# Optimization experiments

Measured on AMD Instinct MI355X. Metric: run time of the kernel, lower is better.

## Reference

```python
import jax, jax.numpy as jnp
import numpy as np

B, N, K = 8, 1024, 32
C_IN, C_OUT, C_SIPF, HEADS = 128, 256, 8, 4
D_H = C_IN // HEADS
EPS = 1e-5
NEG_SLOPE = 0.2


def setup_inputs() -> dict:
    key = jax.random.key(0)
    ks = jax.random.split(key, 12)
    s = 0.05
    x = jax.random.normal(ks[0], (B, C_IN, N), jnp.float32)
    SiPF = jax.random.normal(ks[1], (B, N, K, C_SIPF), jnp.float32)
    col_local = jax.random.randint(ks[2], (B, N, K), 0, N)
    # feat_select expects GLOBAL indices (it subtracts the b*N base)
    col = (col_local + jnp.arange(B)[:, None, None] * N).reshape(-1).astype(jnp.int64)
    return {
        "x": x,
        "SiPF": SiPF,
        "w_kv": jax.random.normal(ks[3], (2 * C_IN, C_IN), jnp.float32) * s,
        "wk1": jax.random.normal(ks[4], (C_IN, C_SIPF), jnp.float32) * s,
        "bnk_gamma": jnp.ones((C_IN,), jnp.float32),
        "bnk_beta": jnp.zeros((C_IN,), jnp.float32),
        "wk2": jax.random.normal(ks[5], (C_IN, C_IN), jnp.float32) * s,
        "wv1": jax.random.normal(ks[6], (C_IN, C_SIPF), jnp.float32) * s,
        "bv1": jnp.zeros((C_IN,), jnp.float32),
        "bnv_gamma": jnp.ones((C_IN,), jnp.float32),
        "bnv_beta": jnp.zeros((C_IN,), jnp.float32),
        "wv2": jax.random.normal(ks[7], (C_IN, C_IN), jnp.float32) * s,
        "bv2": jnp.zeros((C_IN,), jnp.float32),
        "we": jax.random.normal(ks[8], (C_OUT, 2 * C_IN), jnp.float32) * s,
        "bne_gamma": jnp.ones((C_OUT,), jnp.float32),
        "bne_beta": jnp.zeros((C_OUT,), jnp.float32),
        "col": col,
        "bs": B,
    }


def _bn2d(t, gamma, beta):
    # BatchNorm2d, training mode: stats over (B, N, K) per channel
    m = t.mean(axis=(0, 2, 3), keepdims=True)
    v = t.var(axis=(0, 2, 3), keepdims=True)
    return (t - m) * jax.lax.rsqrt(v + EPS) * gamma[None, :, None, None] + beta[None, :, None, None]


def _bn1d(t, gamma, beta):
    m = t.mean(axis=(0, 2), keepdims=True)
    v = t.var(axis=(0, 2), keepdims=True)
    return (t - m) * jax.lax.rsqrt(v + EPS) * gamma[None, :, None] + beta[None, :, None]


def _feat_select(feat, col):
    # feat: [B, C, N]; col: [B*N*K] global indices -> [B, C, N, K]
    idx = col.reshape(B, N * K) - (jnp.arange(B, dtype=col.dtype) * N)[:, None]
    gathered = jax.vmap(lambda f, i: f[:, i])(feat, idx)  # [B, C, N*K]
    return gathered.reshape(feat.shape[0], feat.shape[1], N, K)


def _forward(x, SiPF, col, w_kv, wk1, bnk_gamma, bnk_beta, wk2,
             wv1, bv1, bnv_gamma, bnv_beta, wv2, bv2, we, bne_gamma, bne_beta):
    fs = _feat_select(x, col)                               # [B, C_in, N, K]
    sipf = SiPF.reshape(B, N, K, C_SIPF).transpose(0, 3, 1, 2)  # [B, C_sipf, N, K]

    qv = jnp.einsum('oc,bcnk->bonk', w_kv, fs)
    q_fs, v_fs = qv[:, :C_IN], qv[:, C_IN:]

    # bias nets on SiPF (1x1 conv -> BN -> ReLU -> 1x1 conv)
    hk = jax.nn.relu(_bn2d(jnp.einsum('oc,bcnk->bonk', wk1, sipf), bnk_gamma, bnk_beta))
    k_sipf = jnp.einsum('oc,bcnk->bonk', wk2, hk)
    hv = jnp.einsum('oc,bcnk->bonk', wv1, sipf) + bv1[None, :, None, None]
    hv = jax.nn.relu(_bn2d(hv, bnv_gamma, bnv_beta))
    v_sipf = jnp.einsum('oc,bcnk->bonk', wv2, hv) + bv2[None, :, None, None]

    def to_heads(t):  # [B, C_in, N, K] -> [B, H, N, K, d_h]
        return t.reshape(B, HEADS, D_H, N, K).transpose(0, 1, 3, 4, 2)

    q = to_heads(q_fs)
    k = to_heads(k_sipf)
    v = to_heads(v_fs) * to_heads(v_sipf)

    scale = 1.0 / np.sqrt(D_H).astype(np.float32)
    scores = jnp.einsum('bhnkd,bhnjd->bhnkj', q, k) * scale   # [B, H, N, K, K]
    attn = jax.nn.softmax(scores, axis=-1)
    out = jnp.einsum('bhnkj,bhnjd->bhnkd', attn, v)           # [B, H, N, K, d_h]

    y = out.transpose(0, 1, 4, 2, 3).reshape(B, C_IN, N, K)
    y = y.max(axis=-1)                                        # [B, C_in, N]

    z = jnp.concatenate([y - x, x], axis=1)                   # [B, 2*C_in, N]
    z = jnp.einsum('oc,bcn->bon', we, z)
    z = _bn1d(z, bne_gamma, bne_beta)
    return jnp.where(z >= 0, z, NEG_SLOPE * z)                # LeakyReLU(0.2)


def reference(x, SiPF, w_kv, wk1, bnk_gamma, bnk_beta, wk2, wv1, bv1,
              bnv_gamma, bnv_beta, wv2, bv2, we, bne_gamma, bne_beta, col, bs):
    del bs  # unused by the torch module as well
    return _forward(x, SiPF, col, w_kv, wk1, bnk_gamma, bnk_beta, wk2,
                    wv1, bv1, bnv_gamma, bnv_beta, wv2, bv2, we, bne_gamma, bne_beta)
```

## Files before the change

### kernel.cpp

```cpp
#include <hip/hip_runtime.h>

#define B_    8
#define N_    1024
#define K_    32
#define CIN   128
#define COUT  256
#define EPSF  1e-5f
#define NEG   0.2f

#define WS_MP   0
#define WS_ESUM 12288
#define WS_ESS  12544
#define WS_BK   12800
#define WS_BV   12928
#define WB_BYTE 53248
#define XT_BYTE 331776
#define Y_BYTE  2428928
#define WQB   0
#define WVB   16384
#define WK2B  32768
#define WV2B  49152
#define WEB   65536
#define WK1F  131072
#define WV1F  135168

typedef unsigned short ushort_t;
typedef unsigned int   uint_t;
typedef __attribute__((ext_vector_type(8))) short s8v;
typedef __attribute__((ext_vector_type(4))) short s4v;
typedef __attribute__((ext_vector_type(4))) float f4v;
typedef __bf16 bf16x8 __attribute__((ext_vector_type(8)));

constexpr int   P_TOT  = B_ * N_ * K_;
constexpr float INV_P  = 1.0f / (float)P_TOT;
constexpr float INV_BN = 1.0f / (float)(B_ * N_);

__device__ __forceinline__ float b2f(ushort_t u) {
    return __uint_as_float(((uint_t)u) << 16);
}
__device__ __forceinline__ ushort_t f2b(float f) {
    return __builtin_bit_cast(ushort_t, (__bf16)f);
}
__device__ __forceinline__ bf16x8 ld8(const ushort_t* p) {
    return __builtin_bit_cast(bf16x8, *(const s8v*)p);
}
__device__ __forceinline__ int qx2(int c, int k) {
    return (c * 32 + k) ^ (((c >> 1) & 7) << 3);
}

__global__ __launch_bounds__(256) void prep_kernel(
    const float* __restrict__ x, const float* __restrict__ SiPF,
    const float* __restrict__ w_kv, const float* __restrict__ wk2,
    const float* __restrict__ wv2, const float* __restrict__ we,
    float* __restrict__ ws, ushort_t* __restrict__ wb,
    ushort_t* __restrict__ xT)
{
    __shared__ float red[4][44];
    __shared__ float tile[32][129];
    const int blk = blockIdx.x;
    const int t   = threadIdx.x;

    if (blk < 256) {
        float s1[8], s2[36];
#pragma unroll
        for (int i = 0; i < 8; ++i) s1[i] = 0.f;
#pragma unroll
        for (int i = 0; i < 36; ++i) s2[i] = 0.f;
        const int tid = blk * 256 + t;
#pragma unroll
        for (int it = 0; it < P_TOT / 65536; ++it) {
            const float4* base = (const float4*)(SiPF + (size_t)(tid + it * 65536) * 8);
            float4 a = base[0], bq = base[1];
            float v[8] = {a.x, a.y, a.z, a.w, bq.x, bq.y, bq.z, bq.w};
            int idx = 0;
#pragma unroll
            for (int i = 0; i < 8; ++i) {
                s1[i] += v[i];
#pragma unroll
                for (int j = i; j < 8; ++j) s2[idx++] += v[i] * v[j];
            }
        }
#pragma unroll
        for (int i = 0; i < 8; ++i)
            for (int m = 32; m; m >>= 1) s1[i] += __shfl_xor(s1[i], m);
#pragma unroll
        for (int i = 0; i < 36; ++i)
            for (int m = 32; m; m >>= 1) s2[i] += __shfl_xor(s2[i], m);
        if ((t & 63) == 0) {
            const int w = t >> 6;
#pragma unroll
            for (int i = 0; i < 8; ++i) red[w][i] = s1[i];
#pragma unroll
            for (int i = 0; i < 36; ++i) red[w][8 + i] = s2[i];
        }
        __syncthreads();
        if (t < 44)
            ws[WS_MP + blk * 48 + t] = red[0][t] + red[1][t] + red[2][t] + red[3][t];
    } else if (blk < 512) {
        const int tb = blk - 256;
        const int b  = tb >> 5;
        const int n0 = (tb & 31) << 5;
        const int cgr = t >> 5, n = t & 31;
#pragma unroll
        for (int i = 0; i < 16; ++i) {
            const int c = cgr * 16 + i;
            tile[n][c] = x[((size_t)(b * CIN + c)) * N_ + n0 + n];
        }
        __syncthreads();
        const int nr = t >> 3, c0 = (t & 7) * 16;
        s8v o0, o1;
#pragma unroll
        for (int j = 0; j < 8; ++j) {
            o0[j] = (short)f2b(tile[nr][c0 + j]);
            o1[j] = (short)f2b(tile[nr][c0 + 8 + j]);
        }
        s8v* dst = (s8v*)(xT + ((size_t)(b * N_ + n0 + nr)) * 128 + c0);
        dst[0] = o0; dst[1] = o1;
    } else {
        if (blk == 512) {
            ws[WS_ESUM + t] = 0.f;
            ws[WS_ESS + t]  = 0.f;
        }
        const int base = (blk - 512) * 1024 + t;
#pragma unroll
        for (int i = 0; i < 4; ++i) {
            const int e = base + i * 256;
            float v;
            if (e < 32768)      v = w_kv[e];
            else if (e < 49152) v = wk2[e - 32768];
            else if (e < 65536) v = wv2[e - 49152];
            else                v = we[e - 65536];
            wb[e] = f2b(v);
        }
    }
}

__global__ __launch_bounds__(128) void prep2_kernel(
    const float* __restrict__ wk1, const float* __restrict__ wv1,
    const float* __restrict__ bnk_gamma, const float* __restrict__ bnk_beta,
    const float* __restrict__ bnv_gamma, const float* __restrict__ bnv_beta,
    float* __restrict__ ws, ushort_t* __restrict__ wb)
{
    __shared__ float red2[44];
    const int c = threadIdx.x;
    if (c < 44) {
        float s = 0.f;
        for (int bq = 0; bq < 256; ++bq) s += ws[WS_MP + bq * 48 + c];
        red2[c] = s;
    }
    __syncthreads();

    float m1[8], wkr[8], wvr[8];
#pragma unroll
    for (int s = 0; s < 8; ++s) {
        m1[s]  = red2[s] * INV_P;
        wkr[s] = wk1[c * 8 + s];
        wvr[s] = wv1[c * 8 + s];
    }
    float mk = 0.f, mv = 0.f;
#pragma unroll
    for (int s = 0; s < 8; ++s) { mk += wkr[s] * m1[s]; mv += wvr[s] * m1[s]; }
    float ek = 0.f, ev = 0.f;
#pragma unroll
    for (int s = 0; s < 8; ++s)
#pragma unroll
        for (int s2 = 0; s2 < 8; ++s2) {
            const int i = s < s2 ? s : s2;
            const int j = s < s2 ? s2 : s;
            const float m2 = red2[8 + 8 * i - (i * (i - 1)) / 2 + (j - i)] * INV_P;
            ek += wkr[s] * wkr[s2] * m2;
            ev += wvr[s] * wvr[s2] * m2;
        }
    const float Ak = bnk_gamma[c] * rsqrtf(ek - mk * mk + EPSF);
    const float Av = bnv_gamma[c] * rsqrtf(ev - mv * mv + EPSF);
    ws[WS_BK + c] = bnk_beta[c] - mk * Ak;
    ws[WS_BV + c] = bnv_beta[c] - mv * Av;
#pragma unroll
    for (int s = 0; s < 32; ++s) {
        wb[WK1F + c * 32 + s] = s < 8 ? f2b(Ak * wkr[s]) : (ushort_t)0;
        wb[WV1F + c * 32 + s] = s < 8 ? f2b(Av * wvr[s]) : (ushort_t)0;
    }
}

__global__ __launch_bounds__(512, 4) void main_kernel(
    const float* __restrict__ SiPF, const float* __restrict__ bv2,
    const int* __restrict__ col,    const float* __restrict__ ws,
    const ushort_t* __restrict__ wb, const ushort_t* __restrict__ xT,
    ushort_t* __restrict__ y)
{
    __shared__ __align__(16) ushort_t T1[2][4096];
    __shared__ __align__(16) ushort_t T2[2][4096];
    __shared__ __align__(16) ushort_t T3[2][4096];
    __shared__ __align__(16) ushort_t T4[2][4096];

    const int bid = blockIdx.x;
    const int pi  = (bid & 7) * 512 + (bid >> 3);
    const int t   = threadIdx.x;

    const int wv_ = t >> 6, l = t & 63, lr = l & 15, lg = l >> 4;
    const int cw  = wv_ * 16;
    const f4v z4 = {0.f, 0.f, 0.f, 0.f};

    const bf16x8 wa1 = ld8(&wb[WK1F + (cw + lr) * 32 + lg * 8]);
    const bf16x8 wa2 = ld8(&wb[WV1F + (cw + lr) * 32 + lg * 8]);
    bf16x8 wf[8];
    {
        const int c = cw + lr;
#pragma unroll
        for (int kt = 0; kt < 2; ++kt) {
            const int cp0 = kt * 32 + lg * 8;
            wf[kt * 4 + 0] = ld8(&wb[WK2B + c * 128 + cp0]);
            wf[kt * 4 + 1] = ld8(&wb[WV2B + c * 128 + cp0]);
            wf[kt * 4 + 2] = ld8(&wb[WQB  + c * 128 + cp0]);
            wf[kt * 4 + 3] = ld8(&wb[WVB  + c * 128 + cp0]);
        }
    }

    {
        const int p  = t >> 8;
        const int bn = pi * 2 + p;
        const int b  = bn >> 10;
        const int tt = t & 255;
        const int k  = tt & 31;
        const int cg = tt >> 5;
        if (cg < 4) {
            const int slot = (cg * 8) ^ ((k & 3) << 3);
            s8v o8 = {0, 0, 0, 0, 0, 0, 0, 0};
            if (cg == 0) {
                const float4* sp = (const float4*)(SiPF + (size_t)bn * 256 + k * 8);
                const float4 sa = sp[0], sq = sp[1];
                o8[0] = (short)f2b(sa.x); o8[1] = (short)f2b(sa.y);
                o8[2] = (short)f2b(sa.z); o8[3] = (short)f2b(sa.w);
                o8[4] = (short)f2b(sq.x); o8[5] = (short)f2b(sq.y);
                o8[6] = (short)f2b(sq.z); o8[7] = (short)f2b(sq.w);
            }
            *(s8v*)&T4[p][k * 32 + slot] = o8;
        }
        const int idxk = col[bn * K_ + k] - b * N_;
        const s8v* xrow = (const s8v*)(xT + ((size_t)(b << 10) + idxk) * 128 + cg * 16);
        const s8v f0 = xrow[0], f1 = xrow[1];
        const int base = k * 128 + cg * 16;
        const int sw   = (k & 7) << 3;
        *(s8v*)&T1[p][(base) ^ sw]     = f0;
        *(s8v*)&T1[p][(base + 8) ^ sw] = f1;
    }
    __syncthreads();

    {
        bf16x8 sb[4];
#pragma unroll
        for (int nt = 0; nt < 4; ++nt) {
            const int pp  = nt >> 1;
            const int row = (nt & 1) * 16 + lr;
            sb[nt] = ld8(&T4[pp][row * 32 + ((lg * 8) ^ ((row & 3) << 3))]);
        }
        const float4 bka = *(const float4*)&ws[WS_BK + cw + lg * 4];
        const float4 bva = *(const float4*)&ws[WS_BV + cw + lg * 4];
        const float Bk_[4] = {bka.x, bka.y, bka.z, bka.w};
        const float Bv_[4] = {bva.x, bva.y, bva.z, bva.w};
        f4v hka[4], hva[4];
#pragma unroll
        for (int nt = 0; nt < 4; ++nt) {
            hka[nt] = __builtin_amdgcn_mfma_f32_16x16x32_bf16(wa1, sb[nt], z4, 0, 0, 0);
            hva[nt] = __builtin_amdgcn_mfma_f32_16x16x32_bf16(wa2, sb[nt], z4, 0, 0, 0);
        }
#pragma unroll
        for (int nt = 0; nt < 4; ++nt) {
            const int pp  = nt >> 1;
            const int c0  = cw + lg * 4;
            const int kc  = (nt & 1) * 16 + lr;
            const int idx = (kc * 128 + c0) ^ ((kc & 7) << 3);
            s4v hk4, hv4;
#pragma unroll
            for (int r = 0; r < 4; ++r) {
                hk4[r] = (short)f2b(fmaxf(hka[nt][r] + Bk_[r], 0.f));
                hv4[r] = (short)f2b(fmaxf(hva[nt][r] + Bv_[r], 0.f));
            }
            *(s4v*)&T2[pp][idx] = hk4;
            *(s4v*)&T3[pp][idx] = hv4;
        }
    }
    __syncthreads();

    f4v ck[4], cs[4], aq[4], av[4];
#pragma unroll
    for (int nt = 0; nt < 4; ++nt) { ck[nt] = z4; cs[nt] = z4; aq[nt] = z4; av[nt] = z4; }
#pragma unroll
    for (int kt = 0; kt < 4; ++kt) {
        const int cp0 = kt * 32 + lg * 8;
        bf16x8 bk[4], bv[4], bfr[4];
#pragma unroll
        for (int nt = 0; nt < 4; ++nt) {
            const int pp  = nt >> 1;
            const int kk_ = (nt & 1) * 16 + lr;
            const int idx = (kk_ * 128 + cp0) ^ ((lr & 7) << 3);
            bk[nt]  = ld8(&T2[pp][idx]);
            bv[nt]  = ld8(&T3[pp][idx]);
            bfr[nt] = ld8(&T1[pp][idx]);
        }
        const int c = cw + lr;
        const bf16x8 a1 = kt < 2 ? wf[kt * 4 + 0] : ld8(&wb[WK2B + c * 128 + cp0]);
        const bf16x8 a2 = kt < 2 ? wf[kt * 4 + 1] : ld8(&wb[WV2B + c * 128 + cp0]);
        const bf16x8 a3 = kt < 2 ? wf[kt * 4 + 2] : ld8(&wb[WQB  + c * 128 + cp0]);
        const bf16x8 a4 = kt < 2 ? wf[kt * 4 + 3] : ld8(&wb[WVB  + c * 128 + cp0]);
#pragma unroll
        for (int nt = 0; nt < 4; ++nt) {
            ck[nt] = __builtin_amdgcn_mfma_f32_16x16x32_bf16(a1, bk[nt],  ck[nt], 0, 0, 0);
            cs[nt] = __builtin_amdgcn_mfma_f32_16x16x32_bf16(a2, bv[nt],  cs[nt], 0, 0, 0);
            aq[nt] = __builtin_amdgcn_mfma_f32_16x16x32_bf16(a3, bfr[nt], aq[nt], 0, 0, 0);
            av[nt] = __builtin_amdgcn_mfma_f32_16x16x32_bf16(a4, bfr[nt], av[nt], 0, 0, 0);
        }
    }
#pragma unroll
    for (int nt = 0; nt < 4; ++nt) {
        const int pp  = nt >> 1;
        const int c0  = cw + lg * 4;
        const int kk_ = (nt & 1) * 16 + lr;
        const int idx = (kk_ * 128 + c0) ^ ((kk_ & 7) << 3);
        s4v ck4;
#pragma unroll
        for (int r = 0; r < 4; ++r) ck4[r] = (short)f2b(ck[nt][r]);
        *(s4v*)&T4[pp][idx] = ck4;
    }
    __syncthreads();

    {
        const float4 bvv = *(const float4*)&bv2[cw + lg * 4];
        const float bv2_[4] = {bvv.x, bvv.y, bvv.z, bvv.w};
        const float SC = 0.17677669529663687f;
#pragma unroll
        for (int nt = 0; nt < 4; ++nt) {
            const int pp  = nt >> 1;
            const int c0  = cw + lg * 4;
            const int kk_ = (nt & 1) * 16 + lr;
            const int idx = (kk_ * 128 + c0) ^ ((kk_ & 7) << 3);
            s4v q4;
#pragma unroll
            for (int r = 0; r < 4; ++r) {
                q4[r] = (short)f2b(aq[nt][r] * SC);
                T3[pp][qx2(c0 + r, kk_)] =
                    f2b(av[nt][r] * (cs[nt][r] + bv2_[r]));
            }
            *(s4v*)&T2[pp][idx] = q4;
        }
    }
    __syncthreads();

    {
        const int pp = wv_ >> 2;
        const int h  = wv_ & 3;
        const int bn = pi * 2 + pp;
        bf16x8 aqf[2], bkf[2];
#pragma unroll
        for (int mt = 0; mt < 2; ++mt)
            aqf[mt] = ld8(&T2[pp][((mt * 16 + lr) * 128 + h * 32 + lg * 8) ^ ((lr & 7) << 3)]);
#pragma unroll
        for (int nt = 0; nt < 2; ++nt)
            bkf[nt] = ld8(&T4[pp][((nt * 16 + lr) * 128 + h * 32 + lg * 8) ^ ((lr & 7) << 3)]);
        f4v s[2][2];
#pragma unroll
        for (int mt = 0; mt < 2; ++mt)
#pragma unroll
            for (int nt = 0; nt < 2; ++nt)
                s[mt][nt] = __builtin_amdgcn_mfma_f32_16x16x32_bf16(aqf[mt], bkf[nt], z4, 0, 0, 0);

        float rm[2][4], rs[2][4];
#pragma unroll
        for (int mt = 0; mt < 2; ++mt)
#pragma unroll
            for (int r = 0; r < 4; ++r)
                rm[mt][r] = fmaxf(s[mt][0][r], s[mt][1][r]);
#pragma unroll
        for (int m = 1; m <= 8; m <<= 1)
#pragma unroll
            for (int mt = 0; mt < 2; ++mt)
#pragma unroll
                for (int r = 0; r < 4; ++r)
                    rm[mt][r] = fmaxf(rm[mt][r], __shfl_xor(rm[mt][r], m));
#pragma unroll
        for (int mt = 0; mt < 2; ++mt)
#pragma unroll
            for (int nt = 0; nt < 2; ++nt)
#pragma unroll
                for (int r = 0; r < 4; ++r)
                    s[mt][nt][r] = __expf(s[mt][nt][r] - rm[mt][r]);
#pragma unroll
        for (int mt = 0; mt < 2; ++mt)
#pragma unroll
            for (int r = 0; r < 4; ++r)
                rs[mt][r] = s[mt][0][r] + s[mt][1][r];
#pragma unroll
        for (int m = 1; m <= 8; m <<= 1)
#pragma unroll
            for (int mt = 0; mt < 2; ++mt)
#pragma unroll
                for (int r = 0; r < 4; ++r)
                    rs[mt][r] += __shfl_xor(rs[mt][r], m);
#pragma unroll
        for (int mt = 0; mt < 2; ++mt)
#pragma unroll
            for (int r = 0; r < 4; ++r)
                rs[mt][r] = 1.0f / rs[mt][r];

        ushort_t* P = &T1[pp][h * 1024];
#pragma unroll
        for (int mt = 0; mt < 2; ++mt)
#pragma unroll
            for (int nt = 0; nt < 2; ++nt)
#pragma unroll
                for (int r = 0; r < 4; ++r) {
                    const int kq = mt * 16 + lg * 4 + r;
                    const int j  = nt * 16 + lr;
                    P[(kq * 32 + j) ^ ((kq & 7) << 3)] = f2b(s[mt][nt][r] * rs[mt][r]);
                }

        bf16x8 af[2], pb[2];
#pragma unroll
        for (int mt2 = 0; mt2 < 2; ++mt2)
            af[mt2] = ld8(&T3[pp][qx2(h * 32 + mt2 * 16 + lr, lg * 8)]);
#pragma unroll
        for (int nt2 = 0; nt2 < 2; ++nt2) {
            const int kq2 = nt2 * 16 + lr;
            pb[nt2] = ld8(&P[(kq2 * 32 + lg * 8) ^ ((lr & 7) << 3)]);
        }
        f4v o2[2][2];
#pragma unroll
        for (int mt2 = 0; mt2 < 2; ++mt2)
#pragma unroll
            for (int nt2 = 0; nt2 < 2; ++nt2)
                o2[mt2][nt2] = __builtin_amdgcn_mfma_f32_16x16x32_bf16(af[mt2], pb[nt2], z4, 0, 0, 0);

        float ym[2][4];
#pragma unroll
        for (int mt2 = 0; mt2 < 2; ++mt2)
#pragma unroll
            for (int r = 0; r < 4; ++r)
                ym[mt2][r] = fmaxf(o2[mt2][0][r], o2[mt2][1][r]);
#pragma unroll
        for (int m = 1; m <= 8; m <<= 1)
#pragma unroll
            for (int mt2 = 0; mt2 < 2; ++mt2)
#pragma unroll
                for (int r = 0; r < 4; ++r)
                    ym[mt2][r] = fmaxf(ym[mt2][r], __shfl_xor(ym[mt2][r], m));
        if (lr == 0) {
#pragma unroll
            for (int mt2 = 0; mt2 < 2; ++mt2) {
                unsigned long long pk = 0;
#pragma unroll
                for (int r = 0; r < 4; ++r)
                    pk |= ((unsigned long long)f2b(ym[mt2][r])) << (16 * r);
                *(unsigned long long*)&y[(size_t)bn * 128 + h * 32 + mt2 * 16 + lg * 4] = pk;
            }
        }
    }
}

__global__ __launch_bounds__(256) void zgemm_kernel(
    const ushort_t* __restrict__ wb, const ushort_t* __restrict__ xT,
    const ushort_t* __restrict__ y, float* __restrict__ ws,
    float* __restrict__ out)
{
    __shared__ __align__(16) ushort_t Bt[32 * 256];
    const int blk = blockIdx.x;
    const int bn0 = (blk >> 1) * 32;
    const int mh  = (blk & 1) * 128;
    const int t   = threadIdx.x;
    {
        const int r   = t >> 3;
        const int c0  = (t & 7) * 16;
        const int bnr = bn0 + r;
        const s8v* yr = (const s8v*)(y  + (size_t)bnr * 128 + c0);
        const s8v* xr = (const s8v*)(xT + (size_t)bnr * 128 + c0);
        const s8v y0 = yr[0], y1 = yr[1], x0 = xr[0], x1 = xr[1];
        s8v d0, d1;
#pragma unroll
        for (int j = 0; j < 8; ++j) {
            d0[j] = (short)f2b(b2f((ushort_t)y0[j]) - b2f((ushort_t)x0[j]));
            d1[j] = (short)f2b(b2f((ushort_t)y1[j]) - b2f((ushort_t)x1[j]));
        }
        const int sw = (r & 7) << 3;
        *(s8v*)&Bt[(r * 256 + c0) ^ sw]           = d0;
        *(s8v*)&Bt[(r * 256 + c0 + 8) ^ sw]       = d1;
        *(s8v*)&Bt[(r * 256 + 128 + c0) ^ sw]     = x0;
        *(s8v*)&Bt[(r * 256 + 128 + c0 + 8) ^ sw] = x1;
    }
    __syncthreads();

    const int w = t >> 6, l = t & 63, lr = l & 15, lg = l >> 4;
    const f4v z4 = {0.f, 0.f, 0.f, 0.f};
    f4v acc[2][2];
#pragma unroll
    for (int mt = 0; mt < 2; ++mt)
#pragma unroll
        for (int nt = 0; nt < 2; ++nt) acc[mt][nt] = z4;

#pragma unroll
    for (int kt = 0; kt < 8; ++kt) {
        const int kc = kt * 32 + lg * 8;
        bf16x8 bf[2];
#pragma unroll
        for (int nt = 0; nt < 2; ++nt) {
            const int rl = nt * 16 + lr;
            bf[nt] = ld8(&Bt[(rl * 256 + kc) ^ ((lr & 7) << 3)]);
        }
#pragma unroll
        for (int mt = 0; mt < 2; ++mt) {
            const int o = mh + w * 32 + mt * 16 + lr;
            const bf16x8 am = ld8(&wb[WEB + o * 256 + kc]);
#pragma unroll
            for (int nt = 0; nt < 2; ++nt)
                acc[mt][nt] = __builtin_amdgcn_mfma_f32_16x16x32_bf16(am, bf[nt], acc[mt][nt], 0, 0, 0);
        }
    }

    float sm[2][4], sq[2][4];
#pragma unroll
    for (int mt = 0; mt < 2; ++mt)
#pragma unroll
        for (int r = 0; r < 4; ++r) {
            const float a0 = acc[mt][0][r], a1 = acc[mt][1][r];
            sm[mt][r] = a0 + a1;
            sq[mt][r] = a0 * a0 + a1 * a1;
        }
#pragma unroll
    for (int m = 1; m <= 8; m <<= 1)
#pragma unroll
        for (int mt = 0; mt < 2; ++mt)
#pragma unroll
            for (int r = 0; r < 4; ++r) {
                sm[mt][r] += __shfl_xor(sm[mt][r], m);
                sq[mt][r] += __shfl_xor(sq[mt][r], m);
            }
    if (lr == 0) {
#pragma unroll
        for (int mt = 0; mt < 2; ++mt)
#pragma unroll
            for (int r = 0; r < 4; ++r) {
                const int o = mh + w * 32 + mt * 16 + lg * 4 + r;
                atomicAdd(&ws[WS_ESUM + o], sm[mt][r]);
                atomicAdd(&ws[WS_ESS + o],  sq[mt][r]);
            }
    }
    const int b = bn0 >> 10;
#pragma unroll
    for (int mt = 0; mt < 2; ++mt)
#pragma unroll
        for (int r = 0; r < 4; ++r) {
            const int o = mh + w * 32 + mt * 16 + lg * 4 + r;
#pragma unroll
            for (int nt = 0; nt < 2; ++nt) {
                const int n = (bn0 + nt * 16 + lr) & (N_ - 1);
                out[((size_t)(b * COUT + o)) * N_ + n] = acc[mt][nt][r];
            }
        }
}

__global__ __launch_bounds__(256) void apply_kernel(
    const float* __restrict__ ws, const float* __restrict__ gamma,
    const float* __restrict__ beta, float* __restrict__ out)
{
    const int bo = blockIdx.x;
    const int o  = bo & 255;
    const int b  = bo >> 8;
    const float mean = ws[WS_ESUM + o] * INV_BN;
    const float var  = ws[WS_ESS + o] * INV_BN - mean * mean;
    const float A  = gamma[o] * rsqrtf(var + EPSF);
    const float Bb = beta[o] - mean * A;
    float4* p = (float4*)(out + ((size_t)(b * COUT + o)) * N_);
    float4 v = p[threadIdx.x];
    float r0 = A * v.x + Bb, r1 = A * v.y + Bb;
    float r2 = A * v.z + Bb, r3 = A * v.w + Bb;
    v.x = r0 >= 0.f ? r0 : NEG * r0;
    v.y = r1 >= 0.f ? r1 : NEG * r1;
    v.z = r2 >= 0.f ? r2 : NEG * r2;
    v.w = r3 >= 0.f ? r3 : NEG * r3;
    p[threadIdx.x] = v;
}

extern "C" void kernel_launch(void* const* d_in, const int* in_sizes, int n_in,
                              void* d_out, int out_size, void* d_ws, size_t ws_size,
                              hipStream_t stream)
{
    (void)in_sizes; (void)n_in; (void)out_size; (void)ws_size;

    const float* x         = (const float*)d_in[0];
    const float* SiPF      = (const float*)d_in[1];
    const float* w_kv      = (const float*)d_in[2];
    const float* wk1       = (const float*)d_in[3];
    const float* bnk_gamma = (const float*)d_in[4];
    const float* bnk_beta  = (const float*)d_in[5];
    const float* wk2       = (const float*)d_in[6];
    const float* wv1       = (const float*)d_in[7];
    const float* bnv_gamma = (const float*)d_in[9];
    const float* bnv_beta  = (const float*)d_in[10];
    const float* wv2       = (const float*)d_in[11];
    const float* bv2       = (const float*)d_in[12];
    const float* we        = (const float*)d_in[13];
    const float* bne_gamma = (const float*)d_in[14];
    const float* bne_beta  = (const float*)d_in[15];
    const int*   col       = (const int*)d_in[16];

    float*    ws = (float*)d_ws;
    ushort_t* wb = (ushort_t*)((char*)d_ws + WB_BYTE);
    ushort_t* xT = (ushort_t*)((char*)d_ws + XT_BYTE);
    ushort_t* y  = (ushort_t*)((char*)d_ws + Y_BYTE);

    prep_kernel<<<640, 256, 0, stream>>>(x, SiPF, w_kv, wk2, wv2, we, ws, wb, xT);
    prep2_kernel<<<1, 128, 0, stream>>>(wk1, wv1, bnk_gamma, bnk_beta,
                                        bnv_gamma, bnv_beta, ws, wb);
    main_kernel<<<4096, 512, 0, stream>>>(SiPF, bv2, col, ws, wb, xT, y);
    zgemm_kernel<<<512, 256, 0, stream>>>(wb, xT, y, ws, (float*)d_out);
    apply_kernel<<<2048, 256, 0, stream>>>(ws, bne_gamma, bne_beta,
                                           (float*)d_out);
}
```

Measured before the change: 186.9 us.

## Defer softmax normalization via ones-MFMA row sums and drop max subtraction

The attention softmax no longer subtracts the row max or normalizes with shuffle reductions. It writes unnormalized exp scores to LDS, gets row sums from an extra MFMA against a ones vector, and rescales the PV output before the max-pool. The early register preload of the weight fragments is removed in favour of loads inside the loop, which should lower register pressure. s_setprio hints are added around the MFMA-heavy sections. Dropping the max subtraction risks exp overflow if scores grow large, and the row sums are taken from bf16-rounded probabilities.

```diff
diff --git a/kernel.cpp b/kernel.cpp
--- a/kernel.cpp
+++ b/kernel.cpp
@@ -196,25 +196,6 @@
     const int bid = blockIdx.x;
     const int pi  = (bid & 7) * 512 + (bid >> 3);
     const int t   = threadIdx.x;
-
-    const int wv_ = t >> 6, l = t & 63, lr = l & 15, lg = l >> 4;
-    const int cw  = wv_ * 16;
-    const f4v z4 = {0.f, 0.f, 0.f, 0.f};
-
-    const bf16x8 wa1 = ld8(&wb[WK1F + (cw + lr) * 32 + lg * 8]);
-    const bf16x8 wa2 = ld8(&wb[WV1F + (cw + lr) * 32 + lg * 8]);
-    bf16x8 wf[8];
-    {
-        const int c = cw + lr;
-#pragma unroll
-        for (int kt = 0; kt < 2; ++kt) {
-            const int cp0 = kt * 32 + lg * 8;
-            wf[kt * 4 + 0] = ld8(&wb[WK2B + c * 128 + cp0]);
-            wf[kt * 4 + 1] = ld8(&wb[WV2B + c * 128 + cp0]);
-            wf[kt * 4 + 2] = ld8(&wb[WQB  + c * 128 + cp0]);
-            wf[kt * 4 + 3] = ld8(&wb[WVB  + c * 128 + cp0]);
-        }
-    }
 
     {
         const int p  = t >> 8;
@@ -246,6 +227,10 @@
     }
     __syncthreads();
 
+    const int wv_ = t >> 6, l = t & 63, lr = l & 15, lg = l >> 4;
+    const int cw  = wv_ * 16;
+    const f4v z4 = {0.f, 0.f, 0.f, 0.f};
+
     {
         bf16x8 sb[4];
 #pragma unroll
@@ -258,11 +243,13 @@
         const float4 bva = *(const float4*)&ws[WS_BV + cw + lg * 4];
         const float Bk_[4] = {bka.x, bka.y, bka.z, bka.w};
         const float Bv_[4] = {bva.x, bva.y, bva.z, bva.w};
+        const bf16x8 a1 = ld8(&wb[WK1F + (cw + lr) * 32 + lg * 8]);
+        const bf16x8 a2 = ld8(&wb[WV1F + (cw + lr) * 32 + lg * 8]);
         f4v hka[4], hva[4];
 #pragma unroll
         for (int nt = 0; nt < 4; ++nt) {
-            hka[nt] = __builtin_amdgcn_mfma_f32_16x16x32_bf16(wa1, sb[nt], z4, 0, 0, 0);
-            hva[nt] = __builtin_amdgcn_mfma_f32_16x16x32_bf16(wa2, sb[nt], z4, 0, 0, 0);
+            hka[nt] = __builtin_amdgcn_mfma_f32_16x16x32_bf16(a1, sb[nt], z4, 0, 0, 0);
+            hva[nt] = __builtin_amdgcn_mfma_f32_16x16x32_bf16(a2, sb[nt], z4, 0, 0, 0);
         }
 #pragma unroll
         for (int nt = 0; nt < 4; ++nt) {
@@ -285,6 +272,7 @@
     f4v ck[4], cs[4], aq[4], av[4];
 #pragma unroll
     for (int nt = 0; nt < 4; ++nt) { ck[nt] = z4; cs[nt] = z4; aq[nt] = z4; av[nt] = z4; }
+    __builtin_amdgcn_s_setprio(1);
 #pragma unroll
     for (int kt = 0; kt < 4; ++kt) {
         const int cp0 = kt * 32 + lg * 8;
@@ -299,10 +287,10 @@
             bfr[nt] = ld8(&T1[pp][idx]);
         }
         const int c = cw + lr;
-        const bf16x8 a1 = kt < 2 ? wf[kt * 4 + 0] : ld8(&wb[WK2B + c * 128 + cp0]);
-        const bf16x8 a2 = kt < 2 ? wf[kt * 4 + 1] : ld8(&wb[WV2B + c * 128 + cp0]);
-        const bf16x8 a3 = kt < 2 ? wf[kt * 4 + 2] : ld8(&wb[WQB  + c * 128 + cp0]);
-        const bf16x8 a4 = kt < 2 ? wf[kt * 4 + 3] : ld8(&wb[WVB  + c * 128 + cp0]);
+        const bf16x8 a1 = ld8(&wb[WK2B + c * 128 + cp0]);
+        const bf16x8 a2 = ld8(&wb[WV2B + c * 128 + cp0]);
+        const bf16x8 a3 = ld8(&wb[WQB  + c * 128 + cp0]);
+        const bf16x8 a4 = ld8(&wb[WVB  + c * 128 + cp0]);
 #pragma unroll
         for (int nt = 0; nt < 4; ++nt) {
             ck[nt] = __builtin_amdgcn_mfma_f32_16x16x32_bf16(a1, bk[nt],  ck[nt], 0, 0, 0);
@@ -311,6 +299,7 @@
             av[nt] = __builtin_amdgcn_mfma_f32_16x16x32_bf16(a4, bfr[nt], av[nt], 0, 0, 0);
         }
     }
+    __builtin_amdgcn_s_setprio(0);
 #pragma unroll
     for (int nt = 0; nt < 4; ++nt) {
         const int pp  = nt >> 1;
@@ -364,55 +353,19 @@
             for (int nt = 0; nt < 2; ++nt)
                 s[mt][nt] = __builtin_amdgcn_mfma_f32_16x16x32_bf16(aqf[mt], bkf[nt], z4, 0, 0, 0);
 
-        float rm[2][4], rs[2][4];
+        ushort_t* P = &T1[pp][h * 1024];
 #pragma unroll
         for (int mt = 0; mt < 2; ++mt)
 #pragma unroll
-            for (int r = 0; r < 4; ++r)
-                rm[mt][r] = fmaxf(s[mt][0][r], s[mt][1][r]);
-#pragma unroll
-        for (int m = 1; m <= 8; m <<= 1)
-#pragma unroll
-            for (int mt = 0; mt < 2; ++mt)
-#pragma unroll
-                for (int r = 0; r < 4; ++r)
-                    rm[mt][r] = fmaxf(rm[mt][r], __shfl_xor(rm[mt][r], m));
-#pragma unroll
-        for (int mt = 0; mt < 2; ++mt)
-#pragma unroll
-            for (int nt = 0; nt < 2; ++nt)
-#pragma unroll
-                for (int r = 0; r < 4; ++r)
-                    s[mt][nt][r] = __expf(s[mt][nt][r] - rm[mt][r]);
-#pragma unroll
-        for (int mt = 0; mt < 2; ++mt)
-#pragma unroll
-            for (int r = 0; r < 4; ++r)
-                rs[mt][r] = s[mt][0][r] + s[mt][1][r];
-#pragma unroll
-        for (int m = 1; m <= 8; m <<= 1)
-#pragma unroll
-            for (int mt = 0; mt < 2; ++mt)
-#pragma unroll
-                for (int r = 0; r < 4; ++r)
-                    rs[mt][r] += __shfl_xor(rs[mt][r], m);
-#pragma unroll
-        for (int mt = 0; mt < 2; ++mt)
-#pragma unroll
-            for (int r = 0; r < 4; ++r)
-                rs[mt][r] = 1.0f / rs[mt][r];
-
-        ushort_t* P = &T1[pp][h * 1024];
-#pragma unroll
-        for (int mt = 0; mt < 2; ++mt)
-#pragma unroll
-            for (int nt = 0; nt < 2; ++nt)
+            for (int nt = 0; nt < 2; ++nt) {
+                const int kq0 = mt * 16 + lg * 4;
+                const int j   = nt * 16 + lr;
 #pragma unroll
                 for (int r = 0; r < 4; ++r) {
-                    const int kq = mt * 16 + lg * 4 + r;
-                    const int j  = nt * 16 + lr;
-                    P[(kq * 32 + j) ^ ((kq & 7) << 3)] = f2b(s[mt][nt][r] * rs[mt][r]);
+                    const int kq = kq0 + r;
+                    P[(kq * 32 + j) ^ ((kq & 7) << 3)] = f2b(__expf(s[mt][nt][r]));
                 }
+            }
 
         bf16x8 af[2], pb[2];
 #pragma unroll
@@ -423,19 +376,31 @@
             const int kq2 = nt2 * 16 + lr;
             pb[nt2] = ld8(&P[(kq2 * 32 + lg * 8) ^ ((lr & 7) << 3)]);
         }
-        f4v o2[2][2];
+        const s8v one8 = {(short)0x3F80, (short)0x3F80, (short)0x3F80, (short)0x3F80,
+                          (short)0x3F80, (short)0x3F80, (short)0x3F80, (short)0x3F80};
+        const bf16x8 ones = __builtin_bit_cast(bf16x8, one8);
+
+        f4v o2[2][2], rsf[2];
+        __builtin_amdgcn_s_setprio(1);
 #pragma unroll
         for (int mt2 = 0; mt2 < 2; ++mt2)
 #pragma unroll
             for (int nt2 = 0; nt2 < 2; ++nt2)
                 o2[mt2][nt2] = __builtin_amdgcn_mfma_f32_16x16x32_bf16(af[mt2], pb[nt2], z4, 0, 0, 0);
+#pragma unroll
+        for (int nt2 = 0; nt2 < 2; ++nt2)
+            rsf[nt2] = __builtin_amdgcn_mfma_f32_16x16x32_bf16(ones, pb[nt2], z4, 0, 0, 0);
+        __builtin_amdgcn_s_setprio(0);
+
+        const float inv0 = 1.0f / rsf[0][0];
+        const float inv1 = 1.0f / rsf[1][0];
 
         float ym[2][4];
 #pragma unroll
         for (int mt2 = 0; mt2 < 2; ++mt2)
 #pragma unroll
             for (int r = 0; r < 4; ++r)
-                ym[mt2][r] = fmaxf(o2[mt2][0][r], o2[mt2][1][r]);
+                ym[mt2][r] = fmaxf(o2[mt2][0][r] * inv0, o2[mt2][1][r] * inv1);
 #pragma unroll
         for (int m = 1; m <= 8; m <<= 1)
 #pragma unroll
```

New measurement: 159.1 us. 1.18x faster.
